# Performance work log

Hardware: AMD Instinct MI355X
Metric: run time of the kernel (lower is better)

The kernel has to match this reference:

```python
import jax, jax.numpy as jnp
import numpy as np
from jax import lax


def setup_inputs() -> dict:
    key = jax.random.key(0)
    k1, k2 = jax.random.split(key)
    B, C, H, W = 4, 32, 512, 512
    x = jax.random.normal(k1, (B, C, H, W), dtype=jnp.float32)
    # offset conv params: out_ch = 2*k*k = 18 (init: small weights, zero bias)
    w_off = jax.random.normal(k2, (18, C, 3, 3), dtype=jnp.float32) * 0.05
    b_off = jnp.zeros((18,), dtype=jnp.float32)
    return {"x": x, "w_off": w_off, "b_off": b_off}


def _grid_sample_bilinear_zeros(x, grid):
    # x: (B,C,H,W); grid: (B,H,W,2) in [-1,1], align_corners=True, zeros padding
    B, C, H, W = x.shape
    ix = (grid[..., 0] + 1.0) * 0.5 * (W - 1)  # (B,H,W)
    iy = (grid[..., 1] + 1.0) * 0.5 * (H - 1)
    x0 = jnp.floor(ix); y0 = jnp.floor(iy)
    x1 = x0 + 1.0;      y1 = y0 + 1.0
    wx1 = ix - x0; wx0 = 1.0 - wx1
    wy1 = iy - y0; wy0 = 1.0 - wy1
    bi = jnp.arange(B)[:, None, None]

    def corner(yc, xc, w):
        valid = (xc >= 0) & (xc <= W - 1) & (yc >= 0) & (yc <= H - 1)
        xi = jnp.clip(xc, 0, W - 1).astype(jnp.int32)
        yi = jnp.clip(yc, 0, H - 1).astype(jnp.int32)
        v = x[bi, :, yi, xi]  # (B,H,W,C)
        return v * (w * valid.astype(x.dtype))[..., None]

    out = (corner(y0, x0, wy0 * wx0) + corner(y0, x1, wy0 * wx1)
           + corner(y1, x0, wy1 * wx0) + corner(y1, x1, wy1 * wx1))
    return out.transpose(0, 3, 1, 2)  # (B,C,H,W)


def reference(x, w_off, b_off):
    B, C, H, W = x.shape
    # offset conv: 3x3, stride 1, padding 1 (shape-preserving)
    off = lax.conv_general_dilated(
        x, w_off, window_strides=(1, 1), padding=((1, 1), (1, 1)),
        dimension_numbers=("NCHW", "OIHW", "NCHW"))
    off = off + b_off[None, :, None, None]               # (B,18,H,W)
    off = off.transpose(0, 2, 3, 1).reshape(B, H, W, 9, 2)
    # base integer grid: (x, y) per pixel
    gy, gx = jnp.meshgrid(jnp.arange(H, dtype=x.dtype),
                          jnp.arange(W, dtype=x.dtype), indexing="ij")
    base = jnp.stack([gx, gy], axis=-1)                  # (H,W,2)
    g = base[None, :, :, None, :] + off                  # (B,H,W,9,2)
    g = g / jnp.array([W - 1, H - 1], dtype=x.dtype) * 2.0 - 1.0
    g = g[:, :, :, 0, :]                                 # only first kernel offset used
    return _grid_sample_bilinear_zeros(x, g)
```

## Files before the change

kernel.cpp:

```cpp
#include <hip/hip_runtime.h>

#define BB 4
#define CC 32
#define HH 512
#define WW 512
#define PLANE ((size_t)HH * WW)
#define NPIX ((size_t)BB * HH * WW)

__global__ __launch_bounds__(256) void conv_off_kernel(
    const float* __restrict__ x, const float* __restrict__ w_off,
    const float* __restrict__ b_off, float* __restrict__ off) {
  const int t  = threadIdx.x;
  const int w4 = (t & 127) << 2;
  const int h  = blockIdx.y * 2 + (t >> 7);
  const int b  = blockIdx.z;

  float4 acc0, acc1;
  {
    const float b0 = b_off[0], b1 = b_off[1];
    acc0.x = acc0.y = acc0.z = acc0.w = b0;
    acc1.x = acc1.y = acc1.z = acc1.w = b1;
  }

  const float* xr = x + (size_t)b * CC * PLANE + (size_t)h * WW + w4;
  const float* wp0 = w_off;
  const float* wp1 = w_off + 288;

  for (int ci = 0; ci < CC; ++ci) {
#pragma unroll
    for (int kh = 0; kh < 3; ++kh) {
      const int hy = h + kh - 1;
      float vl, v0, v1, v2, v3, vr;
      if (hy >= 0 && hy < HH) {
        const float* p = xr + (ptrdiff_t)(kh - 1) * WW;
        const float4 m = *(const float4*)p;
        vl = (w4 > 0) ? p[-1] : 0.f;
        vr = (w4 < WW - 4) ? p[4] : 0.f;
        v0 = m.x; v1 = m.y; v2 = m.z; v3 = m.w;
      } else {
        vl = v0 = v1 = v2 = v3 = vr = 0.f;
      }
      const float a0 = wp0[kh * 3 + 0], a1 = wp0[kh * 3 + 1], a2 = wp0[kh * 3 + 2];
      const float c0 = wp1[kh * 3 + 0], c1 = wp1[kh * 3 + 1], c2 = wp1[kh * 3 + 2];
      acc0.x += vl * a0 + v0 * a1 + v1 * a2;
      acc0.y += v0 * a0 + v1 * a1 + v2 * a2;
      acc0.z += v1 * a0 + v2 * a1 + v3 * a2;
      acc0.w += v2 * a0 + v3 * a1 + vr * a2;
      acc1.x += vl * c0 + v0 * c1 + v1 * c2;
      acc1.y += v0 * c0 + v1 * c1 + v2 * c2;
      acc1.z += v1 * c0 + v2 * c1 + v3 * c2;
      acc1.w += v2 * c0 + v3 * c1 + vr * c2;
    }
    wp0 += 9;
    wp1 += 9;
    xr += PLANE;
  }

  const size_t idx = ((size_t)b * HH + h) * WW + w4;
  *(float4*)(off + idx) = acc0;
  *(float4*)(off + NPIX + idx) = acc1;
}

__global__ __launch_bounds__(256) void sample_kernel(
    const float* __restrict__ x, const float* __restrict__ off,
    float* __restrict__ out) {
  const size_t tid = (size_t)blockIdx.x * 256 + threadIdx.x;
  const int w = (int)(tid & (WW - 1));
  const int h = (int)((tid >> 9) & (HH - 1));
  const int b = (int)(tid >> 18);

  const float ix = (float)w + off[tid];
  const float iy = (float)h + off[NPIX + tid];

  const float x0f = floorf(ix);
  const float y0f = floorf(iy);

  const float wx1 = ix - x0f;
  const float wx0 = 1.f - wx1;
  const float wy1 = iy - y0f;
  const float wy0 = 1.f - wy1;

  const bool vx0 = (x0f >= 0.f) && (x0f <= (float)(WW - 1));
  const bool vx1 = (x0f + 1.f >= 0.f) && (x0f + 1.f <= (float)(WW - 1));
  const bool vy0 = (y0f >= 0.f) && (y0f <= (float)(HH - 1));
  const bool vy1 = (y0f + 1.f >= 0.f) && (y0f + 1.f <= (float)(HH - 1));

  const int xi0 = (int)fminf(fmaxf(x0f, 0.f), (float)(WW - 1));
  const int xi1 = (int)fminf(fmaxf(x0f + 1.f, 0.f), (float)(WW - 1));
  const int yi0 = (int)fminf(fmaxf(y0f, 0.f), (float)(HH - 1));
  const int yi1 = (int)fminf(fmaxf(y0f + 1.f, 0.f), (float)(HH - 1));

  const float w00 = wy0 * wx0 * ((vy0 && vx0) ? 1.f : 0.f);
  const float w01 = wy0 * wx1 * ((vy0 && vx1) ? 1.f : 0.f);
  const float w10 = wy1 * wx0 * ((vy1 && vx0) ? 1.f : 0.f);
  const float w11 = wy1 * wx1 * ((vy1 && vx1) ? 1.f : 0.f);

  const int i00 = yi0 * WW + xi0;
  const int i01 = yi0 * WW + xi1;
  const int i10 = yi1 * WW + xi0;
  const int i11 = yi1 * WW + xi1;

  const float* xp = x + (size_t)b * CC * PLANE;
  float* ob = out + (size_t)b * CC * PLANE + (size_t)h * WW + w;

#pragma unroll 8
  for (int c = 0; c < CC; ++c) {
    const float v = w00 * xp[i00] + w01 * xp[i01] + w10 * xp[i10] + w11 * xp[i11];
    __builtin_nontemporal_store(v, ob);
    xp += PLANE;
    ob += PLANE;
  }
}

extern "C" void kernel_launch(void* const* d_in, const int* in_sizes, int n_in,
                              void* d_out, int out_size, void* d_ws, size_t ws_size,
                              hipStream_t stream) {
  const float* x     = (const float*)d_in[0];
  const float* w_off = (const float*)d_in[1];
  const float* b_off = (const float*)d_in[2];
  float* out = (float*)d_out;
  float* off = (float*)d_ws;

  dim3 gridA(1, HH / 2, BB);
  conv_off_kernel<<<gridA, 256, 0, stream>>>(x, w_off, b_off, off);

  const int nblk = (int)(NPIX / 256);
  sample_kernel<<<nblk, 256, 0, stream>>>(x, off, out);
}
```

Measured before the change: 351.9 us.

## Compute two output rows per thread in offset conv and swizzle blocks across XCDs

Each conv thread now computes two adjacent output rows, loading four input rows per channel instead of three per row, so vertically overlapping rows are reused from registers. Block indices in both kernels are remapped so that consecutive logical tiles land on the same XCD, which is meant to improve L2 locality for neighbouring rows across the MI355X's chiplets. The conv grid drops to 512 blocks, which lowers parallelism and raises register use per thread.

```diff
diff --git a/kernel.cpp b/kernel.cpp
--- a/kernel.cpp
+++ b/kernel.cpp
@@ -10,61 +10,89 @@
 __global__ __launch_bounds__(256) void conv_off_kernel(
     const float* __restrict__ x, const float* __restrict__ w_off,
     const float* __restrict__ b_off, float* __restrict__ off) {
+  const int nb = gridDim.x;
+  const int i  = blockIdx.x;
+  const int j  = (i & 7) * (nb >> 3) + (i >> 3);
+  const int b    = j >> 7;
+  const int row0 = (j & 127) << 2;
+
   const int t  = threadIdx.x;
   const int w4 = (t & 127) << 2;
-  const int h  = blockIdx.y * 2 + (t >> 7);
-  const int b  = blockIdx.z;
+  const int h0 = row0 + ((t >> 7) << 1);
 
-  float4 acc0, acc1;
+  float4 a0v, a1v, b0v, b1v;
   {
     const float b0 = b_off[0], b1 = b_off[1];
-    acc0.x = acc0.y = acc0.z = acc0.w = b0;
-    acc1.x = acc1.y = acc1.z = acc1.w = b1;
+    a0v.x = a0v.y = a0v.z = a0v.w = b0;  b0v = a0v;
+    a1v.x = a1v.y = a1v.z = a1v.w = b1;  b1v = a1v;
   }
 
-  const float* xr = x + (size_t)b * CC * PLANE + (size_t)h * WW + w4;
+  const float* xb = x + (size_t)b * CC * PLANE + (size_t)h0 * WW + w4;
   const float* wp0 = w_off;
   const float* wp1 = w_off + 288;
 
   for (int ci = 0; ci < CC; ++ci) {
+    float vl[4], vr[4], v0[4], v1[4], v2[4], v3[4];
+#pragma unroll
+    for (int r = 0; r < 4; ++r) {
+      const int hy = h0 - 1 + r;
+      if (hy >= 0 && hy < HH) {
+        const float* p = xb + (ptrdiff_t)(r - 1) * WW;
+        const float4 m = *(const float4*)p;
+        vl[r] = (w4 > 0) ? p[-1] : 0.f;
+        vr[r] = (w4 < WW - 4) ? p[4] : 0.f;
+        v0[r] = m.x; v1[r] = m.y; v2[r] = m.z; v3[r] = m.w;
+      } else {
+        vl[r] = vr[r] = v0[r] = v1[r] = v2[r] = v3[r] = 0.f;
+      }
+    }
 #pragma unroll
     for (int kh = 0; kh < 3; ++kh) {
-      const int hy = h + kh - 1;
-      float vl, v0, v1, v2, v3, vr;
-      if (hy >= 0 && hy < HH) {
-        const float* p = xr + (ptrdiff_t)(kh - 1) * WW;
-        const float4 m = *(const float4*)p;
-        vl = (w4 > 0) ? p[-1] : 0.f;
-        vr = (w4 < WW - 4) ? p[4] : 0.f;
-        v0 = m.x; v1 = m.y; v2 = m.z; v3 = m.w;
-      } else {
-        vl = v0 = v1 = v2 = v3 = vr = 0.f;
-      }
       const float a0 = wp0[kh * 3 + 0], a1 = wp0[kh * 3 + 1], a2 = wp0[kh * 3 + 2];
       const float c0 = wp1[kh * 3 + 0], c1 = wp1[kh * 3 + 1], c2 = wp1[kh * 3 + 2];
-      acc0.x += vl * a0 + v0 * a1 + v1 * a2;
-      acc0.y += v0 * a0 + v1 * a1 + v2 * a2;
-      acc0.z += v1 * a0 + v2 * a1 + v3 * a2;
-      acc0.w += v2 * a0 + v3 * a1 + vr * a2;
-      acc1.x += vl * c0 + v0 * c1 + v1 * c2;
-      acc1.y += v0 * c0 + v1 * c1 + v2 * c2;
-      acc1.z += v1 * c0 + v2 * c1 + v3 * c2;
-      acc1.w += v2 * c0 + v3 * c1 + vr * c2;
+      {
+        const int r = kh;
+        a0v.x += vl[r] * a0 + v0[r] * a1 + v1[r] * a2;
+        a0v.y += v0[r] * a0 + v1[r] * a1 + v2[r] * a2;
+        a0v.z += v1[r] * a0 + v2[r] * a1 + v3[r] * a2;
+        a0v.w += v2[r] * a0 + v3[r] * a1 + vr[r] * a2;
+        a1v.x += vl[r] * c0 + v0[r] * c1 + v1[r] * c2;
+        a1v.y += v0[r] * c0 + v1[r] * c1 + v2[r] * c2;
+        a1v.z += v1[r] * c0 + v2[r] * c1 + v3[r] * c2;
+        a1v.w += v2[r] * c0 + v3[r] * c1 + vr[r] * c2;
+      }
+      {
+        const int r = kh + 1;
+        b0v.x += vl[r] * a0 + v0[r] * a1 + v1[r] * a2;
+        b0v.y += v0[r] * a0 + v1[r] * a1 + v2[r] * a2;
+        b0v.z += v1[r] * a0 + v2[r] * a1 + v3[r] * a2;
+        b0v.w += v2[r] * a0 + v3[r] * a1 + vr[r] * a2;
+        b1v.x += vl[r] * c0 + v0[r] * c1 + v1[r] * c2;
+        b1v.y += v0[r] * c0 + v1[r] * c1 + v2[r] * c2;
+        b1v.z += v1[r] * c0 + v2[r] * c1 + v3[r] * c2;
+        b1v.w += v2[r] * c0 + v3[r] * c1 + vr[r] * c2;
+      }
     }
     wp0 += 9;
     wp1 += 9;
-    xr += PLANE;
+    xb += PLANE;
   }
 
-  const size_t idx = ((size_t)b * HH + h) * WW + w4;
-  *(float4*)(off + idx) = acc0;
-  *(float4*)(off + NPIX + idx) = acc1;
+  const size_t idx = ((size_t)b * HH + h0) * WW + w4;
+  *(float4*)(off + idx) = a0v;
+  *(float4*)(off + idx + WW) = b0v;
+  *(float4*)(off + NPIX + idx) = a1v;
+  *(float4*)(off + NPIX + idx + WW) = b1v;
 }
 
 __global__ __launch_bounds__(256) void sample_kernel(
     const float* __restrict__ x, const float* __restrict__ off,
     float* __restrict__ out) {
-  const size_t tid = (size_t)blockIdx.x * 256 + threadIdx.x;
+  const int nb = gridDim.x;
+  const int i  = blockIdx.x;
+  const int j  = (i & 7) * (nb >> 3) + (i >> 3);
+  const size_t tid = (size_t)j * 256 + threadIdx.x;
+
   const int w = (int)(tid & (WW - 1));
   const int h = (int)((tid >> 9) & (HH - 1));
   const int b = (int)(tid >> 18);
@@ -121,8 +149,7 @@
   float* out = (float*)d_out;
   float* off = (float*)d_ws;
 
-  dim3 gridA(1, HH / 2, BB);
-  conv_off_kernel<<<gridA, 256, 0, stream>>>(x, w_off, b_off, off);
+  conv_off_kernel<<<512, 256, 0, stream>>>(x, w_off, b_off, off);
 
   const int nblk = (int)(NPIX / 256);
   sample_kernel<<<nblk, 256, 0, stream>>>(x, off, out);
```

After: 340.5 us. -3.3%, faster.

## Fuse offset conv and bilinear sampling into one kernel with 4-pixel vector stores

Applied to the files above, without the earlier changes.

Merges the offset-conv kernel and the sampling kernel into one, so the offset tensor is never written to or read back from global memory and one launch disappears. Each thread now samples 4 adjacent pixels and writes float4 nontemporal stores. Channel loads in the conv are double-buffered, and block indices are remapped so that neighbouring blocks are spread across the grid. The trade-off is more registers per thread and fewer, larger blocks, which may lower occupancy and latency hiding for the scattered gathers.

```diff
diff --git a/kernel.cpp b/kernel.cpp
--- a/kernel.cpp
+++ b/kernel.cpp
@@ -5,15 +5,21 @@
 #define HH 512
 #define WW 512
 #define PLANE ((size_t)HH * WW)
-#define NPIX ((size_t)BB * HH * WW)
 
-__global__ __launch_bounds__(256) void conv_off_kernel(
+typedef float vfloat4 __attribute__((ext_vector_type(4)));
+
+__global__ __launch_bounds__(256) void fused_kernel(
     const float* __restrict__ x, const float* __restrict__ w_off,
-    const float* __restrict__ b_off, float* __restrict__ off) {
-  const int t  = threadIdx.x;
-  const int w4 = (t & 127) << 2;
-  const int h  = blockIdx.y * 2 + (t >> 7);
-  const int b  = blockIdx.z;
+    const float* __restrict__ b_off, float* __restrict__ out) {
+  const int nb = gridDim.x;
+  const int i  = blockIdx.x;
+  const int j  = (i & 7) * (nb >> 3) + (i >> 3);
+  const int b  = j >> 8;
+  const int h  = ((j & 255) << 1) + (threadIdx.x >> 7);
+  const int w4 = (threadIdx.x & 127) << 2;
+
+  const float* xb = x + (size_t)b * CC * PLANE;
+  const float* xr = xb + (size_t)h * WW + w4;
 
   float4 acc0, acc1;
   {
@@ -22,26 +28,32 @@
     acc1.x = acc1.y = acc1.z = acc1.w = b1;
   }
 
-  const float* xr = x + (size_t)b * CC * PLANE + (size_t)h * WW + w4;
-  const float* wp0 = w_off;
-  const float* wp1 = w_off + 288;
-
-  for (int ci = 0; ci < CC; ++ci) {
+  auto load_ch = [&](int ci, float4* mm, float* el, float* er) {
+    const float* base = xr + (size_t)ci * PLANE;
+#pragma unroll
+    for (int kr = 0; kr < 3; ++kr) {
+      const int hy = h + kr - 1;
+      if (hy >= 0 && hy < HH) {
+        const float* p = base + (ptrdiff_t)(kr - 1) * WW;
+        mm[kr] = *(const float4*)p;
+        el[kr] = (w4 > 0) ? p[-1] : 0.f;
+        er[kr] = (w4 < WW - 4) ? p[4] : 0.f;
+      } else {
+        mm[kr] = make_float4(0.f, 0.f, 0.f, 0.f);
+        el[kr] = 0.f;
+        er[kr] = 0.f;
+      }
+    }
+  };
+  auto fma_ch = [&](int ci, const float4* mm, const float* el, const float* er) {
+    const float* wp0 = w_off + ci * 9;
+    const float* wp1 = w_off + 288 + ci * 9;
 #pragma unroll
     for (int kh = 0; kh < 3; ++kh) {
-      const int hy = h + kh - 1;
-      float vl, v0, v1, v2, v3, vr;
-      if (hy >= 0 && hy < HH) {
-        const float* p = xr + (ptrdiff_t)(kh - 1) * WW;
-        const float4 m = *(const float4*)p;
-        vl = (w4 > 0) ? p[-1] : 0.f;
-        vr = (w4 < WW - 4) ? p[4] : 0.f;
-        v0 = m.x; v1 = m.y; v2 = m.z; v3 = m.w;
-      } else {
-        vl = v0 = v1 = v2 = v3 = vr = 0.f;
-      }
       const float a0 = wp0[kh * 3 + 0], a1 = wp0[kh * 3 + 1], a2 = wp0[kh * 3 + 2];
       const float c0 = wp1[kh * 3 + 0], c1 = wp1[kh * 3 + 1], c2 = wp1[kh * 3 + 2];
+      const float vl = el[kh], vr = er[kh];
+      const float v0 = mm[kh].x, v1 = mm[kh].y, v2 = mm[kh].z, v3 = mm[kh].w;
       acc0.x += vl * a0 + v0 * a1 + v1 * a2;
       acc0.y += v0 * a0 + v1 * a1 + v2 * a2;
       acc0.z += v1 * a0 + v2 * a1 + v3 * a2;
@@ -51,62 +63,67 @@
       acc1.z += v1 * c0 + v2 * c1 + v3 * c2;
       acc1.w += v2 * c0 + v3 * c1 + vr * c2;
     }
-    wp0 += 9;
-    wp1 += 9;
-    xr += PLANE;
+  };
+
+  {
+    float4 mA[3], mB[3];
+    float lA[3], rA[3], lB[3], rB[3];
+    load_ch(0, mA, lA, rA);
+#pragma unroll 4
+    for (int ci = 0; ci < CC; ci += 2) {
+      load_ch(ci + 1, mB, lB, rB);
+      fma_ch(ci, mA, lA, rA);
+      if (ci + 2 < CC) load_ch(ci + 2, mA, lA, rA);
+      fma_ch(ci + 1, mB, lB, rB);
+    }
   }
 
-  const size_t idx = ((size_t)b * HH + h) * WW + w4;
-  *(float4*)(off + idx) = acc0;
-  *(float4*)(off + NPIX + idx) = acc1;
-}
+  int i00[4], i01[4], i10[4], i11[4];
+  float w00[4], w01[4], w10[4], w11[4];
+#pragma unroll
+  for (int p = 0; p < 4; ++p) {
+    const float ox = (p == 0) ? acc0.x : (p == 1) ? acc0.y : (p == 2) ? acc0.z : acc0.w;
+    const float oy = (p == 0) ? acc1.x : (p == 1) ? acc1.y : (p == 2) ? acc1.z : acc1.w;
+    const float ix = (float)(w4 + p) + ox;
+    const float iy = (float)h + oy;
 
-__global__ __launch_bounds__(256) void sample_kernel(
-    const float* __restrict__ x, const float* __restrict__ off,
-    float* __restrict__ out) {
-  const size_t tid = (size_t)blockIdx.x * 256 + threadIdx.x;
-  const int w = (int)(tid & (WW - 1));
-  const int h = (int)((tid >> 9) & (HH - 1));
-  const int b = (int)(tid >> 18);
+    const float x0f = floorf(ix);
+    const float y0f = floorf(iy);
+    const float wx1 = ix - x0f, wx0 = 1.f - wx1;
+    const float wy1 = iy - y0f, wy0 = 1.f - wy1;
 
-  const float ix = (float)w + off[tid];
-  const float iy = (float)h + off[NPIX + tid];
+    const bool vx0 = (x0f >= 0.f) && (x0f <= (float)(WW - 1));
+    const bool vx1 = (x0f + 1.f >= 0.f) && (x0f + 1.f <= (float)(WW - 1));
+    const bool vy0 = (y0f >= 0.f) && (y0f <= (float)(HH - 1));
+    const bool vy1 = (y0f + 1.f >= 0.f) && (y0f + 1.f <= (float)(HH - 1));
 
-  const float x0f = floorf(ix);
-  const float y0f = floorf(iy);
+    const int xi0 = (int)fminf(fmaxf(x0f, 0.f), (float)(WW - 1));
+    const int xi1 = (int)fminf(fmaxf(x0f + 1.f, 0.f), (float)(WW - 1));
+    const int yi0 = (int)fminf(fmaxf(y0f, 0.f), (float)(HH - 1));
+    const int yi1 = (int)fminf(fmaxf(y0f + 1.f, 0.f), (float)(HH - 1));
 
-  const float wx1 = ix - x0f;
-  const float wx0 = 1.f - wx1;
-  const float wy1 = iy - y0f;
-  const float wy0 = 1.f - wy1;
+    w00[p] = wy0 * wx0 * ((vy0 && vx0) ? 1.f : 0.f);
+    w01[p] = wy0 * wx1 * ((vy0 && vx1) ? 1.f : 0.f);
+    w10[p] = wy1 * wx0 * ((vy1 && vx0) ? 1.f : 0.f);
+    w11[p] = wy1 * wx1 * ((vy1 && vx1) ? 1.f : 0.f);
 
-  const bool vx0 = (x0f >= 0.f) && (x0f <= (float)(WW - 1));
-  const bool vx1 = (x0f + 1.f >= 0.f) && (x0f + 1.f <= (float)(WW - 1));
-  const bool vy0 = (y0f >= 0.f) && (y0f <= (float)(HH - 1));
-  const bool vy1 = (y0f + 1.f >= 0.f) && (y0f + 1.f <= (float)(HH - 1));
+    i00[p] = yi0 * WW + xi0;
+    i01[p] = yi0 * WW + xi1;
+    i10[p] = yi1 * WW + xi0;
+    i11[p] = yi1 * WW + xi1;
+  }
 
-  const int xi0 = (int)fminf(fmaxf(x0f, 0.f), (float)(WW - 1));
-  const int xi1 = (int)fminf(fmaxf(x0f + 1.f, 0.f), (float)(WW - 1));
-  const int yi0 = (int)fminf(fmaxf(y0f, 0.f), (float)(HH - 1));
-  const int yi1 = (int)fminf(fmaxf(y0f + 1.f, 0.f), (float)(HH - 1));
-
-  const float w00 = wy0 * wx0 * ((vy0 && vx0) ? 1.f : 0.f);
-  const float w01 = wy0 * wx1 * ((vy0 && vx1) ? 1.f : 0.f);
-  const float w10 = wy1 * wx0 * ((vy1 && vx0) ? 1.f : 0.f);
-  const float w11 = wy1 * wx1 * ((vy1 && vx1) ? 1.f : 0.f);
-
-  const int i00 = yi0 * WW + xi0;
-  const int i01 = yi0 * WW + xi1;
-  const int i10 = yi1 * WW + xi0;
-  const int i11 = yi1 * WW + xi1;
-
-  const float* xp = x + (size_t)b * CC * PLANE;
-  float* ob = out + (size_t)b * CC * PLANE + (size_t)h * WW + w;
-
-#pragma unroll 8
+  const float* xp = xb;
+  float* ob = out + (size_t)b * CC * PLANE + (size_t)h * WW + w4;
+#pragma unroll 4
   for (int c = 0; c < CC; ++c) {
-    const float v = w00 * xp[i00] + w01 * xp[i01] + w10 * xp[i10] + w11 * xp[i11];
-    __builtin_nontemporal_store(v, ob);
+    vfloat4 v;
+#pragma unroll
+    for (int p = 0; p < 4; ++p) {
+      v[p] = w00[p] * xp[i00[p]] + w01[p] * xp[i01[p]] +
+             w10[p] * xp[i10[p]] + w11[p] * xp[i11[p]];
+    }
+    __builtin_nontemporal_store(v, (vfloat4*)ob);
     xp += PLANE;
     ob += PLANE;
   }
@@ -119,11 +136,6 @@
   const float* w_off = (const float*)d_in[1];
   const float* b_off = (const float*)d_in[2];
   float* out = (float*)d_out;
-  float* off = (float*)d_ws;
 
-  dim3 gridA(1, HH / 2, BB);
-  conv_off_kernel<<<gridA, 256, 0, stream>>>(x, w_off, b_off, off);
-
-  const int nblk = (int)(NPIX / 256);
-  sample_kernel<<<nblk, 256, 0, stream>>>(x, off, out);
+  fused_kernel<<<1024, 256, 0, stream>>>(x, w_off, b_off, out);
 }
```

Result: no change. 355.7 us (+1.1%).
